# Performance work log

Measured on AMD Instinct MI355X. Metric: run time of the kernel, lower is better.

## Reference

```python
import jax, jax.numpy as jnp
import numpy as np

NC = 80          # num classes
REG_MAX = 16     # DFL bins
STRIDES = (8, 16, 32)
FEAT_HW = ((80, 80), (40, 40), (20, 20))
MAX_DET = 100
CONF_THRES = 0.25
IOU_THRES = 0.45
PRE_TOPK = 1000  # pre-NMS candidate count (EfficientNMS-style preselection)


def setup_inputs() -> dict:
    key = jax.random.key(0)
    k1, k2, k3 = jax.random.split(key, 3)
    B = 32
    no = 4 * REG_MAX + NC  # 144
    return {
        "p3": jax.random.normal(k1, (B, no, 80, 80), dtype=jnp.float32),
        "p4": jax.random.normal(k2, (B, no, 40, 40), dtype=jnp.float32),
        "p5": jax.random.normal(k3, (B, no, 20, 20), dtype=jnp.float32),
    }


def _make_anchors():
    # grid_cell_offset = 0.5, matching ultralytics make_anchors
    pts, strs = [], []
    for (h, w), s in zip(FEAT_HW, STRIDES):
        sx = jnp.arange(w, dtype=jnp.float32) + 0.5
        sy = jnp.arange(h, dtype=jnp.float32) + 0.5
        yy, xx = jnp.meshgrid(sy, sx, indexing="ij")
        pts.append(jnp.stack([xx.ravel(), yy.ravel()], axis=-1))  # [h*w, 2]
        strs.append(jnp.full((h * w, 1), float(s), dtype=jnp.float32))
    return jnp.concatenate(pts, 0), jnp.concatenate(strs, 0)  # [A,2], [A,1]


def _pairwise_iou(b):
    # b: [K, 4] xyxy
    area = (b[:, 2] - b[:, 0]) * (b[:, 3] - b[:, 1])
    lt = jnp.maximum(b[:, None, :2], b[None, :, :2])
    rb = jnp.minimum(b[:, None, 2:], b[None, :, 2:])
    wh = jnp.clip(rb - lt, 0.0)
    inter = wh[..., 0] * wh[..., 1]
    return inter / (area[:, None] + area[None, :] - inter + 1e-7)


def _nms_single(bxyxy, conf):
    # Greedy class-agnostic NMS over PRE_TOPK score-sorted boxes.
    K = bxyxy.shape[0]
    iou = _pairwise_iou(bxyxy)  # [K, K]
    idx = jnp.arange(K)

    def step(suppressed, xs):
        i, row = xs
        keep = jnp.logical_and(jnp.logical_not(suppressed[i]), conf[i] > 0.0)
        suppressed = jnp.logical_or(suppressed, keep & (row > IOU_THRES) & (idx > i))
        return suppressed, keep

    _, keeps = jax.lax.scan(step, jnp.zeros(K, dtype=bool), (idx, iou))
    return keeps  # [K] bool


def reference(p3, p4, p5):
    feats = [p3, p4, p5]
    B = p3.shape[0]
    no = 4 * REG_MAX + NC
    # concat across scales: [B, no, A]
    x_cat = jnp.concatenate([f.reshape(B, no, -1) for f in feats], axis=2)
    box, cls = x_cat[:, : 4 * REG_MAX], x_cat[:, 4 * REG_MAX:]

    anchors, strd = _make_anchors()  # [A,2], [A,1]
    A = box.shape[-1]

    # DFL: softmax over reg_max bins, expectation with arange weights
    prob = jax.nn.softmax(box.reshape(B, 4, REG_MAX, A), axis=2)
    dist = jnp.einsum("bkra,r->bka", prob, jnp.arange(REG_MAX, dtype=jnp.float32))

    # dist2bbox (xywh) then scale by stride
    anc = anchors.T  # [2, A]
    lt, rb = dist[:, :2], dist[:, 2:]
    x1y1 = anc - lt
    x2y2 = anc + rb
    dbox = jnp.concatenate([(x1y1 + x2y2) * 0.5, x2y2 - x1y1], axis=1) * strd.T  # [B,4,A]

    boxes = dbox.transpose(0, 2, 1)                       # [B, A, 4] xywh
    scores = jax.nn.sigmoid(cls).transpose(0, 2, 1)       # [B, A, NC] (score_activation=1)

    # class-agnostic: best class per box
    conf = scores.max(-1)                                 # [B, A]
    cls_id = jnp.argmax(scores, -1)                       # [B, A]
    conf_m = jnp.where(conf > CONF_THRES, conf, -1.0)

    topv, topi = jax.lax.top_k(conf_m, PRE_TOPK)          # [B, K]
    bsel = jnp.take_along_axis(boxes, topi[..., None], axis=1)  # [B, K, 4]
    cx, cy, w, h = bsel[..., 0], bsel[..., 1], bsel[..., 2], bsel[..., 3]
    bxyxy = jnp.stack([cx - w * 0.5, cy - h * 0.5, cx + w * 0.5, cy + h * 0.5], -1)

    keeps = jax.vmap(_nms_single)(bxyxy, topv)            # [B, K]
    kept_scores = jnp.where(keeps, topv, -1.0)
    dv, di = jax.lax.top_k(kept_scores, MAX_DET)          # [B, MAX_DET]
    valid = dv > 0.0

    det_scores = jnp.where(valid, dv, 0.0)
    det_boxes = jnp.take_along_axis(bxyxy, di[..., None], axis=1) * valid[..., None]
    sel_cls = jnp.take_along_axis(jnp.take_along_axis(cls_id, topi, 1), di, 1)
    det_classes = jnp.where(valid, sel_cls, 0).astype(jnp.int32)
    num_dets = valid.sum(-1, keepdims=True).astype(jnp.int32)
    return num_dets, det_boxes, det_scores, det_classes
```

## Files before the change

kernel.cpp:

```cpp
#include <hip/hip_runtime.h>
#include <math.h>

#define NCLS 80
#define NA 8400
#define NB 32
#define NO 144
#define PRE_TOPK 1000
#define MAX_DET 100

template<int HW, int WDIM, int S>
__device__ __forceinline__ void decode_store(
    const float* __restrict__ src, int g, int aoff,
    float* __restrict__ conf, int* __restrict__ clsid, float* __restrict__ box)
{
    int b = g / HW;
    int pos = g - b * HW;
    float ax = (float)(pos % WDIM) + 0.5f;
    float ay = (float)(pos / WDIM) + 0.5f;
    const float* base = src + (size_t)b * (NO * HW) + pos;

    float vd[64];
    #pragma unroll
    for (int i = 0; i < 64; ++i) vd[i] = base[(size_t)i * HW];

    float vc[80];
    #pragma unroll
    for (int c = 0; c < 80; ++c) vc[c] = base[(size_t)(64 + c) * HW];

    float m0 = vc[0];  int i0 = 0;
    float m1 = vc[20]; int i1 = 20;
    float m2 = vc[40]; int i2 = 40;
    float m3 = vc[60]; int i3 = 60;
    #pragma unroll
    for (int c = 1; c < 20; ++c) {
        if (vc[c]      > m0) { m0 = vc[c];      i0 = c;      }
        if (vc[20 + c] > m1) { m1 = vc[20 + c]; i1 = 20 + c; }
        if (vc[40 + c] > m2) { m2 = vc[40 + c]; i2 = 40 + c; }
        if (vc[60 + c] > m3) { m3 = vc[60 + c]; i3 = 60 + c; }
    }
    float m = m0; int bid = i0;
    if (m1 > m) { m = m1; bid = i1; }
    if (m2 > m) { m = m2; bid = i2; }
    if (m3 > m) { m = m3; bid = i3; }
    float conf_v = 1.0f / (1.0f + __expf(-m));

    float dist[4];
    #pragma unroll
    for (int s4 = 0; s4 < 4; ++s4) {
        float mm = vd[s4 * 16];
        #pragma unroll
        for (int r = 1; r < 16; ++r) mm = fmaxf(mm, vd[s4 * 16 + r]);
        float e[16]; float sum = 0.f;
        #pragma unroll
        for (int r = 0; r < 16; ++r) { e[r] = __expf(vd[s4 * 16 + r] - mm); sum += e[r]; }
        float inv = 1.0f / sum;
        float d = 0.f;
        #pragma unroll
        for (int r = 1; r < 16; ++r) d += (e[r] * inv) * (float)r;
        dist[s4] = d;
    }

    float x1 = ax - dist[0], y1 = ay - dist[1];
    float x2 = ax + dist[2], y2 = ay + dist[3];
    float cx = ((x1 + x2) * 0.5f) * (float)S;
    float cy = ((y1 + y2) * 0.5f) * (float)S;
    float w  = (x2 - x1) * (float)S;
    float h  = (y2 - y1) * (float)S;

    size_t gid = (size_t)b * NA + aoff + pos;
    conf[gid]  = conf_v;
    clsid[gid] = bid;
    *(float4*)(box + gid * 4) = make_float4(cx, cy, w, h);
}

__global__ __launch_bounds__(256) void k_decode(
    const float* __restrict__ p3, const float* __restrict__ p4, const float* __restrict__ p5,
    float* __restrict__ conf, int* __restrict__ clsid, float* __restrict__ box)
{
    int blk = blockIdx.x;
    int t = threadIdx.x;
    if (blk < 800) {
        int g = blk * 256 + t;
        decode_store<6400, 80, 8>(p3, g, 0, conf, clsid, box);
    } else if (blk < 1000) {
        int g = (blk - 800) * 256 + t;
        decode_store<1600, 40, 16>(p4, g, 6400, conf, clsid, box);
    } else {
        int g = (blk - 1000) * 256 + t;
        decode_store<400, 20, 32>(p5, g, 8000, conf, clsid, box);
    }
}

__device__ __forceinline__ uint32_t ord_bits(float f) {
    uint32_t u = __float_as_uint(f);
    return (u & 0x80000000u) ? ~u : (u | 0x80000000u);
}

__global__ __launch_bounds__(1024) void k_topk(
    const float* __restrict__ conf, const float* __restrict__ box, const int* __restrict__ clsid,
    float* __restrict__ topv, float* __restrict__ bxyxy, int* __restrict__ topcls)
{
    int b = blockIdx.x;
    int t = threadIdx.x;

    __shared__ uint32_t ob[NA];
    __shared__ uint32_t hist[256];
    __shared__ uint64_t sbuf[1024];
    __shared__ uint64_t s_prefix;
    __shared__ int s_k;
    __shared__ int s_cnt;

    const float* cf = conf + (size_t)b * NA;
    for (int i = t; i < NA; i += 1024) {
        float c = cf[i];
        float cm = (c > 0.25f) ? c : -1.0f;
        ob[i] = ord_bits(cm);
    }
    if (t == 0) { s_prefix = 0; s_k = PRE_TOPK; s_cnt = 0; }
    sbuf[t] = 0;
    __syncthreads();

    for (int pass = 0; pass < 8; ++pass) {
        int shift = 56 - 8 * pass;
        if (t < 256) hist[t] = 0;
        __syncthreads();
        uint64_t prefix = s_prefix;
        int k = s_k;
        for (int i = t; i < NA; i += 1024) {
            uint64_t key = ((uint64_t)ob[i] << 32) | (uint64_t)(0xFFFFFFFFu - (uint32_t)i);
            bool match = (pass == 0) || (((key ^ prefix) >> (64 - 8 * pass)) == 0);
            if (match) atomicAdd(&hist[(uint32_t)(key >> shift) & 255u], 1u);
        }
        __syncthreads();
        if (t < 64) {
            uint32_t h0 = hist[4 * t + 0], h1 = hist[4 * t + 1];
            uint32_t h2 = hist[4 * t + 2], h3 = hist[4 * t + 3];
            uint32_t part = h0 + h1 + h2 + h3;
            uint32_t s = part;
            #pragma unroll
            for (int off = 1; off < 64; off <<= 1) {
                uint32_t v = __shfl_down(s, off);
                if (t + off < 64) s += v;
            }
            uint32_t cb3 = s - part;
            uint32_t cb2 = cb3 + h3;
            uint32_t cb1 = cb2 + h2;
            uint32_t cb0 = cb1 + h1;
            uint32_t ku = (uint32_t)k;
            if (cb3 < ku && ku <= cb3 + h3) { s_k = k - (int)cb3; s_prefix = prefix | ((uint64_t)(uint32_t)(4 * t + 3) << shift); }
            if (cb2 < ku && ku <= cb2 + h2) { s_k = k - (int)cb2; s_prefix = prefix | ((uint64_t)(uint32_t)(4 * t + 2) << shift); }
            if (cb1 < ku && ku <= cb1 + h1) { s_k = k - (int)cb1; s_prefix = prefix | ((uint64_t)(uint32_t)(4 * t + 1) << shift); }
            if (cb0 < ku && ku <= cb0 + h0) { s_k = k - (int)cb0; s_prefix = prefix | ((uint64_t)(uint32_t)(4 * t + 0) << shift); }
        }
        __syncthreads();
    }

    uint64_t kstar = s_prefix;
    for (int i = t; i < NA; i += 1024) {
        uint64_t key = ((uint64_t)ob[i] << 32) | (uint64_t)(0xFFFFFFFFu - (uint32_t)i);
        if (key >= kstar) {
            int p = atomicAdd(&s_cnt, 1);
            if (p < 1024) sbuf[p] = key;
        }
    }
    __syncthreads();

    for (int k = 2; k <= 1024; k <<= 1) {
        for (int j = k >> 1; j > 0; j >>= 1) {
            int ixj = t ^ j;
            if (ixj > t) {
                uint64_t A = sbuf[t], Bv = sbuf[ixj];
                bool descBlock = ((t & k) == 0);
                bool sw = descBlock ? (A < Bv) : (A > Bv);
                if (sw) { sbuf[t] = Bv; sbuf[ixj] = A; }
            }
            __syncthreads();
        }
    }

    if (t < PRE_TOPK) {
        uint64_t key = sbuf[t];
        uint32_t u = (uint32_t)(key >> 32);
        uint32_t fb = (u & 0x80000000u) ? (u ^ 0x80000000u) : ~u;
        float val = __uint_as_float(fb);
        int idx = (int)(0xFFFFFFFFu - (uint32_t)(key & 0xFFFFFFFFull));
        size_t g = (size_t)b * NA + idx;
        float cx = box[g * 4 + 0], cy = box[g * 4 + 1];
        float w  = box[g * 4 + 2], h  = box[g * 4 + 3];
        size_t o = (size_t)b * PRE_TOPK + t;
        topv[o] = val;
        bxyxy[o * 4 + 0] = cx - w * 0.5f;
        bxyxy[o * 4 + 1] = cy - h * 0.5f;
        bxyxy[o * 4 + 2] = cx + w * 0.5f;
        bxyxy[o * 4 + 3] = cy + h * 0.5f;
        topcls[o] = clsid[g];
    }
}

__global__ __launch_bounds__(256) void k_iou(
    const float* __restrict__ bxyxy, unsigned long long* __restrict__ mask)
{
    __shared__ float4 boxes[PRE_TOPK];
    int b = blockIdx.y;
    int t = threadIdx.x;
    const float4* bp = (const float4*)(bxyxy + (size_t)b * PRE_TOPK * 4);
    for (int i = t; i < PRE_TOPK; i += 256) boxes[i] = bp[i];
    __syncthreads();

    int r_local = t >> 4, w = t & 15;
    int row = blockIdx.x * 16 + r_local;
    if (row >= PRE_TOPK) return;

    float4 bi = boxes[row];
    float area_i = (bi.z - bi.x) * (bi.w - bi.y);
    unsigned long long bits = 0;
    int j0 = w * 64;
    #pragma unroll 4
    for (int jj = 0; jj < 64; ++jj) {
        int j = j0 + jj;
        if (j >= PRE_TOPK) break;
        if (j <= row) continue;
        float4 bj = boxes[j];
        float lx = fmaxf(bi.x, bj.x), ly = fmaxf(bi.y, bj.y);
        float rx = fminf(bi.z, bj.z), ry = fminf(bi.w, bj.w);
        float iw = fmaxf(rx - lx, 0.f), ih = fmaxf(ry - ly, 0.f);
        float inter = iw * ih;
        float area_j = (bj.z - bj.x) * (bj.w - bj.y);
        float iou = inter / (area_i + area_j - inter + 1e-7f);
        if (iou > 0.45f) bits |= (1ull << jj);
    }
    mask[((size_t)b * PRE_TOPK + row) * 16 + w] = bits;
}

#define CHUNK 125
__global__ __launch_bounds__(256) void k_nms(
    const unsigned long long* __restrict__ mask, const float* __restrict__ topv,
    const float* __restrict__ bxyxy, const int* __restrict__ topcls,
    float* __restrict__ out)
{
    int b = blockIdx.x;
    int t = threadIdx.x;

    __shared__ unsigned long long mrows[CHUNK * 16];
    __shared__ float sv[PRE_TOPK];
    __shared__ int kept[MAX_DET];
    __shared__ unsigned long long s_supp[16];
    __shared__ int s_cnt;
    __shared__ int s_done;

    for (int i = t; i < PRE_TOPK; i += 256) sv[i] = topv[(size_t)b * PRE_TOPK + i];
    if (t == 0) { s_cnt = 0; s_done = 0; }
    if (t < 16) s_supp[t] = 0;
    __syncthreads();

    for (int c = 0; c < 8; ++c) {
        int base = c * CHUNK;
        for (int i = t; i < CHUNK * 16; i += 256) {
            int row = base + (i >> 4);
            if (row < PRE_TOPK)
                mrows[i] = mask[((size_t)b * PRE_TOPK + row) * 16 + (i & 15)];
        }
        __syncthreads();
        if (t < 64) {
            unsigned long long supp = (t < 16) ? s_supp[t] : 0ull;
            int cnt = s_cnt;
            int end = base + CHUNK;
            for (int i = base; i < end; ++i) {
                int wsel = i >> 6, bit = i & 63;
                int sbit = (int)((supp >> bit) & 1ull);
                sbit = __shfl(sbit, wsel);
                bool keep = (!sbit) && (sv[i] > 0.0f);
                if (keep) {
                    if (t < 16) supp |= mrows[(i - base) * 16 + t];
                    if (t == 0 && cnt < MAX_DET) kept[cnt] = i;
                    ++cnt;
                }
            }
            if (t < 16) s_supp[t] = supp;
            if (t == 0) { s_cnt = cnt; if (cnt >= MAX_DET) s_done = 1; }
        }
        __syncthreads();
        if (s_done) break;
    }

    int cnt = s_cnt; if (cnt > MAX_DET) cnt = MAX_DET;
    if (t == 0) out[b] = (float)cnt;
    if (t < MAX_DET) {
        bool valid = t < cnt;
        float bx0 = 0.f, bx1 = 0.f, bx2 = 0.f, bx3 = 0.f, sc = 0.f, cl = 0.f;
        if (valid) {
            int p = kept[t];
            size_t o = (size_t)b * PRE_TOPK + p;
            sc = sv[p];
            bx0 = bxyxy[o * 4 + 0];
            bx1 = bxyxy[o * 4 + 1];
            bx2 = bxyxy[o * 4 + 2];
            bx3 = bxyxy[o * 4 + 3];
            cl = (float)topcls[o];
        }
        size_t db = 32 + ((size_t)b * MAX_DET + t) * 4;
        out[db + 0] = bx0; out[db + 1] = bx1; out[db + 2] = bx2; out[db + 3] = bx3;
        out[32 + 12800 + (size_t)b * MAX_DET + t] = sc;
        out[32 + 16000 + (size_t)b * MAX_DET + t] = cl;
    }
}

extern "C" void kernel_launch(void* const* d_in, const int* in_sizes, int n_in,
                              void* d_out, int out_size, void* d_ws, size_t ws_size,
                              hipStream_t stream)
{
    const float* p3 = (const float*)d_in[0];
    const float* p4 = (const float*)d_in[1];
    const float* p5 = (const float*)d_in[2];
    float* out = (float*)d_out;

    char* ws = (char*)d_ws;
    size_t off_mask = 0;
    size_t off_conf = off_mask + (size_t)NB * PRE_TOPK * 16 * 8;
    size_t off_cls  = off_conf + (size_t)NB * NA * 4;
    size_t off_box  = off_cls  + (size_t)NB * NA * 4;
    size_t off_topv = off_box  + (size_t)NB * NA * 4 * 4;
    size_t off_topc = off_topv + (size_t)NB * PRE_TOPK * 4;
    size_t off_bx   = off_topc + (size_t)NB * PRE_TOPK * 4;

    unsigned long long* mask = (unsigned long long*)(ws + off_mask);
    float* conf   = (float*)(ws + off_conf);
    int*   clsid  = (int*)(ws + off_cls);
    float* box    = (float*)(ws + off_box);
    float* topv   = (float*)(ws + off_topv);
    int*   topcls = (int*)(ws + off_topc);
    float* bxyxy  = (float*)(ws + off_bx);

    k_decode<<<1050, 256, 0, stream>>>(p3, p4, p5, conf, clsid, box);
    k_topk<<<NB, 1024, 0, stream>>>(conf, box, clsid, topv, bxyxy, topcls);
    k_iou<<<dim3((PRE_TOPK + 15) / 16, NB), 256, 0, stream>>>(bxyxy, mask);
    k_nms<<<NB, 256, 0, stream>>>(mask, topv, bxyxy, topcls, out);
}
```

Baseline: 158.9 us.

## Fuse top-k, IoU mask and NMS into one per-image kernel; stream decode loads

Merges the top-k, pairwise IoU and greedy NMS kernels into one 1024-thread block per image. IoU mask rows are computed lazily per chunk in shared memory instead of being written to and read back from global memory. This removes two launches and the global mask round-trip, and NMS can stop early without computing later chunks. The trade-off is that IoU work now runs on only 32 blocks instead of being spread across the GPU. The decode kernel also loads DFL and class logits in smaller groups rather than holding all 144 values, which is meant to cut register pressure.

```diff
diff --git a/kernel.cpp b/kernel.cpp
--- a/kernel.cpp
+++ b/kernel.cpp
@@ -7,6 +7,7 @@
 #define NO 144
 #define PRE_TOPK 1000
 #define MAX_DET 100
+#define CHUNK 125
 
 template<int HW, int WDIM, int S>
 __device__ __forceinline__ void decode_store(
@@ -19,46 +20,37 @@
     float ay = (float)(pos / WDIM) + 0.5f;
     const float* base = src + (size_t)b * (NO * HW) + pos;
 
-    float vd[64];
-    #pragma unroll
-    for (int i = 0; i < 64; ++i) vd[i] = base[(size_t)i * HW];
-
-    float vc[80];
-    #pragma unroll
-    for (int c = 0; c < 80; ++c) vc[c] = base[(size_t)(64 + c) * HW];
-
-    float m0 = vc[0];  int i0 = 0;
-    float m1 = vc[20]; int i1 = 20;
-    float m2 = vc[40]; int i2 = 40;
-    float m3 = vc[60]; int i3 = 60;
-    #pragma unroll
-    for (int c = 1; c < 20; ++c) {
-        if (vc[c]      > m0) { m0 = vc[c];      i0 = c;      }
-        if (vc[20 + c] > m1) { m1 = vc[20 + c]; i1 = 20 + c; }
-        if (vc[40 + c] > m2) { m2 = vc[40 + c]; i2 = 40 + c; }
-        if (vc[60 + c] > m3) { m3 = vc[60 + c]; i3 = 60 + c; }
-    }
-    float m = m0; int bid = i0;
-    if (m1 > m) { m = m1; bid = i1; }
-    if (m2 > m) { m = m2; bid = i2; }
-    if (m3 > m) { m = m3; bid = i3; }
-    float conf_v = 1.0f / (1.0f + __expf(-m));
-
     float dist[4];
     #pragma unroll
     for (int s4 = 0; s4 < 4; ++s4) {
-        float mm = vd[s4 * 16];
-        #pragma unroll
-        for (int r = 1; r < 16; ++r) mm = fmaxf(mm, vd[s4 * 16 + r]);
-        float e[16]; float sum = 0.f;
-        #pragma unroll
-        for (int r = 0; r < 16; ++r) { e[r] = __expf(vd[s4 * 16 + r] - mm); sum += e[r]; }
+        float v[16];
+        #pragma unroll
+        for (int r = 0; r < 16; ++r) v[r] = base[(size_t)(s4 * 16 + r) * HW];
+        float mm = v[0];
+        #pragma unroll
+        for (int r = 1; r < 16; ++r) mm = fmaxf(mm, v[r]);
+        float sum = 0.f;
+        #pragma unroll
+        for (int r = 0; r < 16; ++r) { v[r] = __expf(v[r] - mm); sum += v[r]; }
         float inv = 1.0f / sum;
         float d = 0.f;
         #pragma unroll
-        for (int r = 1; r < 16; ++r) d += (e[r] * inv) * (float)r;
+        for (int r = 1; r < 16; ++r) d += (v[r] * inv) * (float)r;
         dist[s4] = d;
     }
+
+    float best = -INFINITY; int bid = 0;
+    #pragma unroll
+    for (int ch = 0; ch < 4; ++ch) {
+        float vc[20];
+        #pragma unroll
+        for (int c = 0; c < 20; ++c) vc[c] = base[(size_t)(64 + ch * 20 + c) * HW];
+        float m = vc[0]; int ii = 0;
+        #pragma unroll
+        for (int c = 1; c < 20; ++c) if (vc[c] > m) { m = vc[c]; ii = c; }
+        if (m > best) { best = m; bid = ch * 20 + ii; }
+    }
+    float conf_v = 1.0f / (1.0f + __expf(-best));
 
     float x1 = ax - dist[0], y1 = ay - dist[1];
     float x2 = ax + dist[2], y2 = ay + dist[3];
@@ -91,24 +83,35 @@
     }
 }
 
+#define SM_SV    16000
+#define SM_MROWS 20000
+#define SM_KEPT  36000
+#define SM_HIST  36608
+#define SM_SBUF  37632
+#define SM_SIZE  45824
+
 __device__ __forceinline__ uint32_t ord_bits(float f) {
     uint32_t u = __float_as_uint(f);
     return (u & 0x80000000u) ? ~u : (u | 0x80000000u);
 }
 
-__global__ __launch_bounds__(1024) void k_topk(
+__global__ __launch_bounds__(1024) void k_post(
     const float* __restrict__ conf, const float* __restrict__ box, const int* __restrict__ clsid,
-    float* __restrict__ topv, float* __restrict__ bxyxy, int* __restrict__ topcls)
+    float* __restrict__ out)
 {
     int b = blockIdx.x;
     int t = threadIdx.x;
 
-    __shared__ uint32_t ob[NA];
-    __shared__ uint32_t hist[256];
-    __shared__ uint64_t sbuf[1024];
+    __shared__ __align__(16) char smem[SM_SIZE];
     __shared__ uint64_t s_prefix;
     __shared__ int s_k;
     __shared__ int s_cnt;
+    __shared__ int s_done;
+    __shared__ unsigned long long s_supp[16];
+
+    uint32_t* ob   = (uint32_t*)smem;
+    uint32_t* hist = (uint32_t*)(smem + SM_HIST);
+    uint64_t* sbuf = (uint64_t*)(smem + SM_SBUF);
 
     const float* cf = conf + (size_t)b * NA;
     for (int i = t; i < NA; i += 1024) {
@@ -116,7 +119,8 @@
         float cm = (c > 0.25f) ? c : -1.0f;
         ob[i] = ord_bits(cm);
     }
-    if (t == 0) { s_prefix = 0; s_k = PRE_TOPK; s_cnt = 0; }
+    if (t == 0) { s_prefix = 0; s_k = PRE_TOPK; s_cnt = 0; s_done = 0; }
+    if (t < 16) s_supp[t] = 0;
     sbuf[t] = 0;
     __syncthreads();
 
@@ -164,6 +168,7 @@
         }
     }
     __syncthreads();
+    if (t == 0) s_cnt = 0;
 
     for (int k = 2; k <= 1024; k <<= 1) {
         for (int j = k >> 1; j > 0; j >>= 1) {
@@ -178,87 +183,48 @@
         }
     }
 
+    float4* boxes = (float4*)smem;
+    float*  sv    = (float*)(smem + SM_SV);
+    uint64_t* mrows = (uint64_t*)(smem + SM_MROWS);
+    int* kept = (int*)(smem + SM_KEPT);
+
     if (t < PRE_TOPK) {
         uint64_t key = sbuf[t];
         uint32_t u = (uint32_t)(key >> 32);
         uint32_t fb = (u & 0x80000000u) ? (u ^ 0x80000000u) : ~u;
-        float val = __uint_as_float(fb);
+        sv[t] = __uint_as_float(fb);
         int idx = (int)(0xFFFFFFFFu - (uint32_t)(key & 0xFFFFFFFFull));
         size_t g = (size_t)b * NA + idx;
-        float cx = box[g * 4 + 0], cy = box[g * 4 + 1];
-        float w  = box[g * 4 + 2], h  = box[g * 4 + 3];
-        size_t o = (size_t)b * PRE_TOPK + t;
-        topv[o] = val;
-        bxyxy[o * 4 + 0] = cx - w * 0.5f;
-        bxyxy[o * 4 + 1] = cy - h * 0.5f;
-        bxyxy[o * 4 + 2] = cx + w * 0.5f;
-        bxyxy[o * 4 + 3] = cy + h * 0.5f;
-        topcls[o] = clsid[g];
-    }
-}
-
-__global__ __launch_bounds__(256) void k_iou(
-    const float* __restrict__ bxyxy, unsigned long long* __restrict__ mask)
-{
-    __shared__ float4 boxes[PRE_TOPK];
-    int b = blockIdx.y;
-    int t = threadIdx.x;
-    const float4* bp = (const float4*)(bxyxy + (size_t)b * PRE_TOPK * 4);
-    for (int i = t; i < PRE_TOPK; i += 256) boxes[i] = bp[i];
-    __syncthreads();
-
-    int r_local = t >> 4, w = t & 15;
-    int row = blockIdx.x * 16 + r_local;
-    if (row >= PRE_TOPK) return;
-
-    float4 bi = boxes[row];
-    float area_i = (bi.z - bi.x) * (bi.w - bi.y);
-    unsigned long long bits = 0;
-    int j0 = w * 64;
-    #pragma unroll 4
-    for (int jj = 0; jj < 64; ++jj) {
-        int j = j0 + jj;
-        if (j >= PRE_TOPK) break;
-        if (j <= row) continue;
-        float4 bj = boxes[j];
-        float lx = fmaxf(bi.x, bj.x), ly = fmaxf(bi.y, bj.y);
-        float rx = fminf(bi.z, bj.z), ry = fminf(bi.w, bj.w);
-        float iw = fmaxf(rx - lx, 0.f), ih = fmaxf(ry - ly, 0.f);
-        float inter = iw * ih;
-        float area_j = (bj.z - bj.x) * (bj.w - bj.y);
-        float iou = inter / (area_i + area_j - inter + 1e-7f);
-        if (iou > 0.45f) bits |= (1ull << jj);
-    }
-    mask[((size_t)b * PRE_TOPK + row) * 16 + w] = bits;
-}
-
-#define CHUNK 125
-__global__ __launch_bounds__(256) void k_nms(
-    const unsigned long long* __restrict__ mask, const float* __restrict__ topv,
-    const float* __restrict__ bxyxy, const int* __restrict__ topcls,
-    float* __restrict__ out)
-{
-    int b = blockIdx.x;
-    int t = threadIdx.x;
-
-    __shared__ unsigned long long mrows[CHUNK * 16];
-    __shared__ float sv[PRE_TOPK];
-    __shared__ int kept[MAX_DET];
-    __shared__ unsigned long long s_supp[16];
-    __shared__ int s_cnt;
-    __shared__ int s_done;
-
-    for (int i = t; i < PRE_TOPK; i += 256) sv[i] = topv[(size_t)b * PRE_TOPK + i];
-    if (t == 0) { s_cnt = 0; s_done = 0; }
-    if (t < 16) s_supp[t] = 0;
+        float4 bx = *(const float4*)(box + g * 4);
+        float cx = bx.x, cy = bx.y, w = bx.z, h = bx.w;
+        boxes[t] = make_float4(cx - w * 0.5f, cy - h * 0.5f, cx + w * 0.5f, cy + h * 0.5f);
+    }
     __syncthreads();
 
     for (int c = 0; c < 8; ++c) {
         int base = c * CHUNK;
-        for (int i = t; i < CHUNK * 16; i += 256) {
-            int row = base + (i >> 4);
-            if (row < PRE_TOPK)
-                mrows[i] = mask[((size_t)b * PRE_TOPK + row) * 16 + (i & 15)];
+        for (int tt = t; tt < CHUNK * 16; tt += 1024) {
+            int rl = tt >> 4, w = tt & 15;
+            int row = base + rl;
+            unsigned long long bits = 0;
+            float4 bi = boxes[row];
+            float area_i = (bi.z - bi.x) * (bi.w - bi.y);
+            int j0 = w * 64;
+            #pragma unroll 4
+            for (int jj = 0; jj < 64; ++jj) {
+                int j = j0 + jj;
+                if (j >= PRE_TOPK) break;
+                if (j <= row) continue;
+                float4 bj = boxes[j];
+                float lx = fmaxf(bi.x, bj.x), ly = fmaxf(bi.y, bj.y);
+                float rx = fminf(bi.z, bj.z), ry = fminf(bi.w, bj.w);
+                float iw = fmaxf(rx - lx, 0.f), ih = fmaxf(ry - ly, 0.f);
+                float inter = iw * ih;
+                float area_j = (bj.z - bj.x) * (bj.w - bj.y);
+                float iou = inter / (area_i + area_j - inter + 1e-7f);
+                if (iou > 0.45f) bits |= (1ull << jj);
+            }
+            mrows[tt] = bits;
         }
         __syncthreads();
         if (t < 64) {
@@ -290,13 +256,12 @@
         float bx0 = 0.f, bx1 = 0.f, bx2 = 0.f, bx3 = 0.f, sc = 0.f, cl = 0.f;
         if (valid) {
             int p = kept[t];
-            size_t o = (size_t)b * PRE_TOPK + p;
+            float4 bb = boxes[p];
+            bx0 = bb.x; bx1 = bb.y; bx2 = bb.z; bx3 = bb.w;
             sc = sv[p];
-            bx0 = bxyxy[o * 4 + 0];
-            bx1 = bxyxy[o * 4 + 1];
-            bx2 = bxyxy[o * 4 + 2];
-            bx3 = bxyxy[o * 4 + 3];
-            cl = (float)topcls[o];
+            uint64_t key = sbuf[p];
+            int idx = (int)(0xFFFFFFFFu - (uint32_t)(key & 0xFFFFFFFFull));
+            cl = (float)clsid[(size_t)b * NA + idx];
         }
         size_t db = 32 + ((size_t)b * MAX_DET + t) * 4;
         out[db + 0] = bx0; out[db + 1] = bx1; out[db + 2] = bx2; out[db + 3] = bx3;
@@ -315,24 +280,14 @@
     float* out = (float*)d_out;
 
     char* ws = (char*)d_ws;
-    size_t off_mask = 0;
-    size_t off_conf = off_mask + (size_t)NB * PRE_TOPK * 16 * 8;
+    size_t off_conf = 0;
     size_t off_cls  = off_conf + (size_t)NB * NA * 4;
     size_t off_box  = off_cls  + (size_t)NB * NA * 4;
-    size_t off_topv = off_box  + (size_t)NB * NA * 4 * 4;
-    size_t off_topc = off_topv + (size_t)NB * PRE_TOPK * 4;
-    size_t off_bx   = off_topc + (size_t)NB * PRE_TOPK * 4;
-
-    unsigned long long* mask = (unsigned long long*)(ws + off_mask);
-    float* conf   = (float*)(ws + off_conf);
-    int*   clsid  = (int*)(ws + off_cls);
-    float* box    = (float*)(ws + off_box);
-    float* topv   = (float*)(ws + off_topv);
-    int*   topcls = (int*)(ws + off_topc);
-    float* bxyxy  = (float*)(ws + off_bx);
+
+    float* conf  = (float*)(ws + off_conf);
+    int*   clsid = (int*)(ws + off_cls);
+    float* box   = (float*)(ws + off_box);
 
     k_decode<<<1050, 256, 0, stream>>>(p3, p4, p5, conf, clsid, box);
-    k_topk<<<NB, 1024, 0, stream>>>(conf, box, clsid, topv, bxyxy, topcls);
-    k_iou<<<dim3((PRE_TOPK + 15) / 16, NB), 256, 0, stream>>>(bxyxy, mask);
-    k_nms<<<NB, 256, 0, stream>>>(mask, topv, bxyxy, topcls, out);
-}
+    k_post<<<NB, 1024, 0, stream>>>(conf, box, clsid, out);
+}
```

New measurement: 193.2 us. 1.22x slower.
